# Optimization experiments

Measured on AMD Instinct MI355X. Metric: run time of the kernel, lower is better.

## Reference

```python
import jax, jax.numpy as jnp
import numpy as np
import math

DIM = 512
HEADS = 8
DH = DIM // HEADS          # 64 = dim_head
M = 17                     # num_landmarks
PINV_ITERS = 6
RES_K = 33                 # residual depthwise conv kernel (lucidrains default)


def layer_norm(x, g, b, eps=1e-5):
    mu = x.mean(-1, keepdims=True)
    var = ((x - mu) ** 2).mean(-1, keepdims=True)
    return (x - mu) * jax.lax.rsqrt(var + eps) * g + b


def dwconv2d(x, w, b, k):
    # x: [B,C,H,W], w: [C,1,k,k] depthwise
    p = k // 2
    y = jax.lax.conv_general_dilated(x, w, (1, 1), ((p, p), (p, p)),
        dimension_numbers=('NCHW', 'OIHW', 'NCHW'), feature_group_count=x.shape[1])
    return y + b[None, :, None, None]


def moore_penrose_pinv(x, iters=PINV_ITERS):
    ax = jnp.abs(x)
    z = jnp.swapaxes(x, -1, -2) / (jnp.max(ax.sum(-1)) * jnp.max(ax.sum(-2)))
    I = jnp.eye(x.shape[-1], dtype=x.dtype)
    for _ in range(iters):
        xz = x @ z
        z = 0.25 * z @ (13 * I - xz @ (15 * I - xz @ (7 * I - xz)))
    return z


def nystrom_attn(x, qkv_w, out_w, out_b, res_w):
    # lucidrains NystromAttention, eval mode (dropout=identity), return_attn=True
    b, n, _ = x.shape
    pad = (M - n % M) % M
    xp = jnp.pad(x, ((0, 0), (pad, 0), (0, 0)))  # pad at FRONT
    q, k, v = jnp.split(xp @ qkv_w, 3, axis=-1)
    to_heads = lambda t: t.reshape(b, -1, HEADS, DH).transpose(0, 2, 1, 3)  # b h n d
    q, k, v = to_heads(q), to_heads(k), to_heads(v)
    q = q * (DH ** -0.5)
    l = (n + pad) // M
    ql = q.reshape(b, HEADS, M, l, DH).mean(3)  # landmarks b h m d
    kl = k.reshape(b, HEADS, M, l, DH).mean(3)
    a1 = jax.nn.softmax(jnp.einsum('bhid,bhjd->bhij', q, kl), axis=-1)   # [b,h,n,m]
    a2 = jax.nn.softmax(jnp.einsum('bhid,bhjd->bhij', ql, kl), axis=-1)  # [b,h,m,m]
    a3 = jax.nn.softmax(jnp.einsum('bhid,bhjd->bhij', ql, k), axis=-1)   # [b,h,m,n]
    a2i = moore_penrose_pinv(a2)
    left = a1 @ a2i                       # [b,h,n,m]
    out = left @ (a3 @ v)                 # [b,h,n,d]
    # residual depthwise conv over heads, kernel (33,1) along seq
    res = jax.lax.conv_general_dilated(v, res_w, (1, 1), ((RES_K // 2, RES_K // 2), (0, 0)),
        dimension_numbers=('NCHW', 'OIHW', 'NCHW'), feature_group_count=HEADS)
    out = out + res
    out = out.transpose(0, 2, 1, 3).reshape(b, -1, DIM)
    out = out @ out_w + out_b
    attn = left @ a3                      # [b,h,n_pad,n_pad]
    return out[:, -n:], attn


def ppeg(x, H, W, w7, b7, w5, b5, w3, b3):
    B, _, C = x.shape
    cls_t, feat = x[:, :1], x[:, 1:]
    cnn = feat.transpose(0, 2, 1).reshape(B, C, H, W)
    y = dwconv2d(cnn, w7, b7, 7) + cnn + dwconv2d(cnn, w5, b5, 5) + dwconv2d(cnn, w3, b3, 3)
    y = y.reshape(B, C, H * W).transpose(0, 2, 1)
    return jnp.concatenate([cls_t, y], axis=1)


def setup_inputs():
    key = jax.random.key(0)
    ks = jax.random.split(key, 20)
    B, N, IN, NC = 2, 2048, 1024, 2
    s = 0.02
    d = {}
    d['feats'] = jax.random.normal(ks[0], (B, N, IN), jnp.float32)
    d['fc1_w'] = jax.random.normal(ks[1], (IN, DIM), jnp.float32) * s
    d['fc1_b'] = jnp.zeros((DIM,), jnp.float32)
    d['cls_token'] = jax.random.normal(ks[2], (1, 1, DIM), jnp.float32)
    for i, pre in enumerate(['l1', 'l2']):
        o = 3 + i * 3
        d[pre + '_norm_g'] = jnp.ones((DIM,), jnp.float32)
        d[pre + '_norm_b'] = jnp.zeros((DIM,), jnp.float32)
        d[pre + '_qkv_w'] = jax.random.normal(ks[o], (DIM, 3 * DIM), jnp.float32) * s
        d[pre + '_out_w'] = jax.random.normal(ks[o + 1], (DIM, DIM), jnp.float32) * s
        d[pre + '_out_b'] = jnp.zeros((DIM,), jnp.float32)
        d[pre + '_res_w'] = jax.random.normal(ks[o + 2], (HEADS, 1, RES_K, 1), jnp.float32) * s
    for kk, kidx in zip([7, 5, 3], [9, 10, 11]):
        d['ppeg_w%d' % kk] = jax.random.normal(ks[kidx], (DIM, 1, kk, kk), jnp.float32) * s
        d['ppeg_b%d' % kk] = jnp.zeros((DIM,), jnp.float32)
    d['norm_g'] = jnp.ones((DIM,), jnp.float32)
    d['norm_b'] = jnp.zeros((DIM,), jnp.float32)
    d['fc2_w'] = jax.random.normal(ks[12], (DIM, NC), jnp.float32) * s
    d['fc2_b'] = jnp.zeros((NC,), jnp.float32)
    return d


def reference(feats, fc1_w, fc1_b, cls_token,
              l1_norm_g, l1_norm_b, l1_qkv_w, l1_out_w, l1_out_b, l1_res_w,
              l2_norm_g, l2_norm_b, l2_qkv_w, l2_out_w, l2_out_b, l2_res_w,
              ppeg_w7, ppeg_b7, ppeg_w5, ppeg_b5, ppeg_w3, ppeg_b3,
              norm_g, norm_b, fc2_w, fc2_b):
    h = jax.nn.relu(feats @ fc1_w + fc1_b)          # [B,N,512]
    N = h.shape[1]
    Hs = int(math.ceil(math.sqrt(N)))               # square grid side
    add = Hs * Hs - N
    h = jnp.concatenate([h, h[:, :add]], axis=1)    # duplicate-pad to Hs*Hs
    B = h.shape[0]
    h = jnp.concatenate([jnp.broadcast_to(cls_token, (B, 1, DIM)), h], axis=1)
    a1, aw1 = nystrom_attn(layer_norm(h, l1_norm_g, l1_norm_b), l1_qkv_w, l1_out_w, l1_out_b, l1_res_w)
    h = h + a1
    h = ppeg(h, Hs, Hs, ppeg_w7, ppeg_b7, ppeg_w5, ppeg_b5, ppeg_w3, ppeg_b3)
    a2, aw2 = nystrom_attn(layer_norm(h, l2_norm_g, l2_norm_b), l2_qkv_w, l2_out_w, l2_out_b, l2_res_w)
    h = h + a2
    h = layer_norm(h, norm_g, norm_b)[:, 0]
    logits = h @ fc2_w + fc2_b
    return logits, aw1, aw2
```

## Files before the change

### kernel.cpp

```cpp
#include <hip/hip_runtime.h>
#include <math.h>
#include <stdint.h>

#define BATCH 2
#define NIN   1024
#define NSEQ  2048
#define DIMC  512
#define NH    8
#define DHD   64
#define MLM   17
#define LBLK  125
#define SEQ   2117
#define NPAD  2125
#define PAD0  8
#define HS    46
#define NPIX  2116
#define RA    4250
#define AWSZ  ((size_t)BATCH*NH*NPAD*NPAD)

typedef _Float16 half8 __attribute__((ext_vector_type(8)));
typedef float    floatx4 __attribute__((ext_vector_type(4)));

__device__ __forceinline__ void store_hl(_Float16* __restrict__ xh, _Float16* __restrict__ xl,
                                         int c, int ra, float v)
{
    _Float16 hv = (_Float16)v;
    size_t o = ((size_t)(c >> 3) * RA + ra) * 8 + (c & 7);
    xh[o] = hv;
    xl[o] = (_Float16)(v - (float)hv);
}

__global__ void convA_kernel(const float* __restrict__ X, _Float16* __restrict__ hi,
                             _Float16* __restrict__ lo, int R, int K)
{
    int GK = K >> 3;
    size_t idx = (size_t)blockIdx.x * 256 + threadIdx.x;
    if (idx >= (size_t)R * GK) return;
    int r = (int)(idx % R); int gk = (int)(idx / R);
    const float* s = X + (size_t)r * K + gk * 8;
    half8 h, l;
    #pragma unroll
    for (int j = 0; j < 8; ++j) {
        float x = s[j];
        _Float16 hh = (_Float16)x;
        h[j] = hh;
        l[j] = (_Float16)(x - (float)hh);
    }
    *(half8*)(hi + idx * 8) = h;
    *(half8*)(lo + idx * 8) = l;
}

__global__ void convB_kernel(const float* __restrict__ X, _Float16* __restrict__ hi,
                             _Float16* __restrict__ lo, int N, int K)
{
    int GK = K >> 3;
    size_t idx = (size_t)blockIdx.x * 256 + threadIdx.x;
    if (idx >= (size_t)N * GK) return;
    int n = (int)(idx % N); int gk = (int)(idx / N);
    const float* s = X + (size_t)(gk * 8) * N + n;
    half8 h, l;
    #pragma unroll
    for (int j = 0; j < 8; ++j) {
        float x = s[(size_t)j * N];
        _Float16 hh = (_Float16)x;
        h[j] = hh;
        l[j] = (_Float16)(x - (float)hh);
    }
    *(half8*)(hi + idx * 8) = h;
    *(half8*)(lo + idx * 8) = l;
}

__global__ __launch_bounds__(256) void gemm_mfma(
    const _Float16* __restrict__ Ah, const _Float16* __restrict__ Al,
    const _Float16* __restrict__ Bh, const _Float16* __restrict__ Bl,
    const float* __restrict__ bias, float* __restrict__ C,
    int Mn, int Nn, int Kn, int relu)
{
    __shared__ _Float16 sA[2][4][128][8];
    __shared__ _Float16 sB[2][4][128][8];
    const int tid = threadIdx.x;
    const int wv = tid >> 6, ln = tid & 63;
    const int m0 = blockIdx.y * 128, n0 = blockIdx.x * 128;
    const int wm = (wv >> 1) * 64, wn = (wv & 1) * 64;
    const int g = ln >> 4, rr = ln & 15;

    floatx4 acc[4][4];
    #pragma unroll
    for (int m = 0; m < 4; ++m)
        #pragma unroll
        for (int n = 0; n < 4; ++n)
            acc[m][n] = (floatx4){0.f, 0.f, 0.f, 0.f};

    for (int k0 = 0; k0 < Kn; k0 += 32) {
        int gk0 = k0 >> 3;
        #pragma unroll
        for (int q2 = 0; q2 < 8; ++q2) {
            int c = wv + q2 * 4;
            int arr = c >> 3, gg = (c >> 1) & 3, hf = c & 1;
            const _Float16* base = (arr == 0) ? Ah : (arr == 1) ? Al : (arr == 2) ? Bh : Bl;
            int Rdim = (arr < 2) ? Mn : Nn;
            int rg = ((arr < 2) ? m0 : n0) + hf * 64 + ln;
            if (arr < 2 && rg >= Mn) rg = Mn - 1;
            const _Float16* src = base + ((size_t)(gk0 + gg) * Rdim + rg) * 8;
            _Float16* dst = (arr == 0) ? &sA[0][gg][hf * 64][0] :
                            (arr == 1) ? &sA[1][gg][hf * 64][0] :
                            (arr == 2) ? &sB[0][gg][hf * 64][0] :
                                         &sB[1][gg][hf * 64][0];
            __builtin_amdgcn_global_load_lds(
                (__attribute__((address_space(1))) void*)(uintptr_t)src,
                (__attribute__((address_space(3))) void*)dst, 16, 0, 0);
        }
        __syncthreads();

        half8 a_h[4], a_l[4], b_h[4], b_l[4];
        #pragma unroll
        for (int m = 0; m < 4; ++m) {
            a_h[m] = *(const half8*)&sA[0][g][wm + m * 16 + rr][0];
            a_l[m] = *(const half8*)&sA[1][g][wm + m * 16 + rr][0];
        }
        #pragma unroll
        for (int n = 0; n < 4; ++n) {
            b_h[n] = *(const half8*)&sB[0][g][wn + n * 16 + rr][0];
            b_l[n] = *(const half8*)&sB[1][g][wn + n * 16 + rr][0];
        }
        #pragma unroll
        for (int m = 0; m < 4; ++m)
            #pragma unroll
            for (int n = 0; n < 4; ++n) {
                acc[m][n] = __builtin_amdgcn_mfma_f32_16x16x32_f16(a_h[m], b_h[n], acc[m][n], 0, 0, 0);
                acc[m][n] = __builtin_amdgcn_mfma_f32_16x16x32_f16(a_l[m], b_h[n], acc[m][n], 0, 0, 0);
                acc[m][n] = __builtin_amdgcn_mfma_f32_16x16x32_f16(a_h[m], b_l[n], acc[m][n], 0, 0, 0);
            }
        __syncthreads();
    }

    const int rq = ln >> 4;
    #pragma unroll
    for (int n = 0; n < 4; ++n) {
        int col = n0 + wn + n * 16 + rr;
        float bv = bias ? bias[col] : 0.f;
        #pragma unroll
        for (int m = 0; m < 4; ++m) {
            #pragma unroll
            for (int r = 0; r < 4; ++r) {
                int row = m0 + wm + m * 16 + rq * 4 + r;
                if (row < Mn) {
                    float vv = acc[m][n][r] + bv;
                    if (relu) vv = fmaxf(vv, 0.f);
                    C[(size_t)row * Nn + col] = vv;
                }
            }
        }
    }
}

__global__ void buildh_kernel(const float* __restrict__ h0, const float* __restrict__ cls,
                              float* __restrict__ h)
{
    size_t e = (size_t)blockIdx.x*256 + threadIdx.x;
    if (e >= (size_t)BATCH*SEQ*DIMC) return;
    int c = e % DIMC; size_t r = e / DIMC;
    int t = r % SEQ; int b = r / SEQ;
    float val;
    if (t == 0) val = cls[c];
    else {
        int n = t - 1;
        if (n >= NSEQ) n -= NSEQ;
        val = h0[((size_t)(b*NSEQ + n))*DIMC + c];
    }
    h[e] = val;
}

__global__ void ln_pad_kernel(const float* __restrict__ h, const float* __restrict__ g,
                              const float* __restrict__ bta,
                              _Float16* __restrict__ xh, _Float16* __restrict__ xl)
{
    int r = blockIdx.x; int b = blockIdx.y; int t = threadIdx.x;
    int ra = b*NPAD + r;
    if (r < PAD0) {
        store_hl(xh, xl, t, ra, 0.f);
        store_hl(xh, xl, t + 256, ra, 0.f);
        return;
    }
    const float* x = &h[((size_t)(b*SEQ + r-PAD0))*DIMC];
    __shared__ float red[256];
    float x0 = x[t], x1 = x[t+256];
    red[t] = x0 + x1; __syncthreads();
    for (int s=128;s>0;s>>=1){ if(t<s) red[t]+=red[t+s]; __syncthreads(); }
    float mu = red[0] * (1.f/512.f); __syncthreads();
    float d0 = x0-mu, d1 = x1-mu;
    red[t] = d0*d0 + d1*d1; __syncthreads();
    for (int s=128;s>0;s>>=1){ if(t<s) red[t]+=red[t+s]; __syncthreads(); }
    float rstd = 1.0f / sqrtf(red[0]*(1.f/512.f) + 1e-5f);
    store_hl(xh, xl, t,       ra, d0*rstd*g[t]     + bta[t]);
    store_hl(xh, xl, t + 256, ra, d1*rstd*g[t+256] + bta[t+256]);
}

__global__ void split_heads_kernel(const float* __restrict__ qkv, float* __restrict__ q,
                                   float* __restrict__ k, float* __restrict__ v)
{
    size_t idx = (size_t)blockIdx.x*256 + threadIdx.x;
    if (idx >= (size_t)BATCH*NH*NPAD*DHD) return;
    int d = idx % DHD; size_t r = idx / DHD;
    int i = r % NPAD; r /= NPAD;
    int h = r % NH; int b = r / NH;
    size_t src = ((size_t)(b*NPAD + i))*1536 + h*DHD + d;
    q[idx] = qkv[src] * 0.125f;
    k[idx] = qkv[src + 512];
    v[idx] = qkv[src + 1024];
}

__global__ void landmark_kernel(const float* __restrict__ q, const float* __restrict__ k,
                                float* __restrict__ ql, float* __restrict__ kl)
{
    int m = blockIdx.x, h = blockIdx.y, b = blockIdx.z, d = threadIdx.x;
    int bh = b*NH + h;
    size_t base = ((size_t)bh*NPAD + m*LBLK)*DHD + d;
    float sq = 0.f, sk = 0.f;
    for (int r=0;r<LBLK;++r){ sq += q[base + (size_t)r*DHD]; sk += k[base + (size_t)r*DHD]; }
    size_t o = ((size_t)bh*MLM + m)*DHD + d;
    ql[o] = sq / 125.f; kl[o] = sk / 125.f;
}

__global__ void a1_kernel(const float* __restrict__ q, const float* __restrict__ kl,
                          float* __restrict__ a1)
{
    int i = blockIdx.x, h = blockIdx.y, b = blockIdx.z;
    int bh = b*NH + h; int lane = threadIdx.x;
    __shared__ float qrow[64];
    __shared__ float dots[MLM];
    qrow[lane] = q[((size_t)bh*NPAD + i)*DHD + lane];
    __syncthreads();
    if (lane < MLM) {
        const float* krow = &kl[((size_t)bh*MLM + lane)*DHD];
        float acc = 0.f;
        for (int d=0; d<DHD; ++d) acc += qrow[d]*krow[d];
        dots[lane] = acc;
    }
    __syncthreads();
    if (lane < MLM) {
        float mx = -1e30f;
        for (int u=0;u<MLM;++u) mx = fmaxf(mx, dots[u]);
        float s = 0.f;
        for (int u=0;u<MLM;++u) s += expf(dots[u]-mx);
        a1[((size_t)bh*NPAD + i)*MLM + lane] = expf(dots[lane]-mx)/s;
    }
}

__global__ void a2_kernel(const float* __restrict__ ql, const float* __restrict__ kl,
                          float* __restrict__ a2)
{
    int bh = blockIdx.x; int t = threadIdx.x;
    __shared__ float s[MLM*MLM];
    if (t < MLM*MLM) {
        int m = t/MLM, j = t%MLM;
        const float* qr = &ql[((size_t)bh*MLM+m)*DHD];
        const float* kr = &kl[((size_t)bh*MLM+j)*DHD];
        float acc=0.f; for(int d=0;d<DHD;++d) acc += qr[d]*kr[d];
        s[t] = acc;
    }
    __syncthreads();
    if (t < MLM*MLM) {
        int m = t/MLM;
        float mx=-1e30f; for(int u=0;u<MLM;++u) mx=fmaxf(mx, s[m*MLM+u]);
        float sm=0.f; for(int u=0;u<MLM;++u) sm += expf(s[m*MLM+u]-mx);
        a2[(size_t)bh*MLM*MLM + t] = expf(s[t]-mx)/sm;
    }
}

__global__ void a3_kernel(const float* __restrict__ ql, const float* __restrict__ k,
                          float* __restrict__ a3)
{
    int m = blockIdx.x, h = blockIdx.y, b = blockIdx.z;
    int bh = b*NH + h; int tid = threadIdx.x;
    __shared__ float qlrow[64];
    __shared__ float buf[NPAD];
    __shared__ float red[256];
    if (tid < 64) qlrow[tid] = ql[((size_t)bh*MLM+m)*DHD + tid];
    __syncthreads();
    for (int j = tid; j < NPAD; j += 256) {
        const float* kr = &k[((size_t)bh*NPAD + j)*DHD];
        float acc = 0.f;
        for (int d=0; d<DHD; ++d) acc += qlrow[d]*kr[d];
        buf[j] = acc;
    }
    __syncthreads();
    float mx = -1e30f;
    for (int j = tid; j < NPAD; j += 256) mx = fmaxf(mx, buf[j]);
    red[tid] = mx; __syncthreads();
    for (int s=128;s>0;s>>=1){ if(tid<s) red[tid]=fmaxf(red[tid],red[tid+s]); __syncthreads(); }
    mx = red[0]; __syncthreads();
    float sm = 0.f;
    for (int j = tid; j < NPAD; j += 256) sm += expf(buf[j]-mx);
    red[tid] = sm; __syncthreads();
    for (int s=128;s>0;s>>=1){ if(tid<s) red[tid]+=red[tid+s]; __syncthreads(); }
    sm = red[0];
    for (int j = tid; j < NPAD; j += 256)
        a3[((size_t)bh*MLM+m)*NPAD + j] = expf(buf[j]-mx)/sm;
}

__global__ void pinv_scale_kernel(const float* __restrict__ a2, float* __restrict__ scal)
{
    int t = threadIdx.x;
    __shared__ float red[512];
    float rs = -1e30f, cs = -1e30f;
    if (t < BATCH*NH*MLM) {
        int bh = t/MLM, i = t%MLM;
        const float* x = &a2[(size_t)bh*MLM*MLM];
        float r=0.f, c=0.f;
        for (int j=0;j<MLM;++j){ r += fabsf(x[i*MLM+j]); c += fabsf(x[j*MLM+i]); }
        rs = r; cs = c;
    }
    red[t] = rs; __syncthreads();
    for (int s=256;s>0;s>>=1){ if(t<s) red[t]=fmaxf(red[t],red[t+s]); __syncthreads(); }
    float m1 = red[0]; __syncthreads();
    red[t] = cs; __syncthreads();
    for (int s=256;s>0;s>>=1){ if(t<s) red[t]=fmaxf(red[t],red[t+s]); __syncthreads(); }
    if (t==0) scal[0] = 1.f/(m1*red[0]);
}

__global__ void pinv_kernel(const float* __restrict__ a2, const float* __restrict__ scal,
                            float* __restrict__ a2i)
{
    int bh = blockIdx.x; int t = threadIdx.x;
    __shared__ float x[289], z[289], xz[289], w1[289], w2[289];
    int i = t/MLM, j = t%MLM;
    bool act = t < MLM*MLM;
    if (act) x[t] = a2[(size_t)bh*MLM*MLM + t];
    __syncthreads();
    if (act) z[t] = x[j*MLM+i] * scal[0];
    __syncthreads();
    for (int it=0; it<6; ++it) {
        if (act){ float a=0.f; for(int k2=0;k2<MLM;++k2) a += x[i*MLM+k2]*z[k2*MLM+j]; xz[t]=a; }
        __syncthreads();
        if (act){ w1[t] = (i==j?7.f:0.f) - xz[t]; }
        __syncthreads();
        if (act){ float a=0.f; for(int k2=0;k2<MLM;++k2) a += xz[i*MLM+k2]*w1[k2*MLM+j]; w2[t]=a; }
        __syncthreads();
        if (act){ w1[t] = (i==j?15.f:0.f) - w2[t]; }
        __syncthreads();
        if (act){ float a=0.f; for(int k2=0;k2<MLM;++k2) a += xz[i*MLM+k2]*w1[k2*MLM+j]; w2[t]=a; }
        __syncthreads();
        if (act){ w1[t] = (i==j?13.f:0.f) - w2[t]; }
        __syncthreads();
        if (act){ float a=0.f; for(int k2=0;k2<MLM;++k2) a += z[i*MLM+k2]*w1[k2*MLM+j]; w2[t]=0.25f*a; }
        __syncthreads();
        if (act) z[t] = w2[t];
        __syncthreads();
    }
    if (act) a2i[(size_t)bh*MLM*MLM + t] = z[t];
}

__global__ void left_kernel(const float* __restrict__ a1, const float* __restrict__ a2i,
                            float* __restrict__ left)
{
    int bh = blockIdx.z*NH + blockIdx.y;
    __shared__ float zi[289];
    int t = threadIdx.x;
    for (int u=t; u<289; u+=256) zi[u] = a2i[(size_t)bh*289+u];
    __syncthreads();
    int e = blockIdx.x*256 + t;
    if (e < NPAD*MLM) {
        int i = e/MLM, j = e%MLM;
        const float* ar = &a1[((size_t)bh*NPAD + i)*MLM];
        float acc=0.f;
        for (int k2=0;k2<MLM;++k2) acc += ar[k2]*zi[k2*MLM+j];
        left[((size_t)bh*NPAD+i)*MLM + j] = acc;
    }
}

__global__ void a3v_kernel(const float* __restrict__ a3, const float* __restrict__ v,
                           float* __restrict__ a3v)
{
    int m = blockIdx.x, h = blockIdx.y, b = blockIdx.z, d = threadIdx.x;
    int bh = b*NH + h;
    const float* ar = &a3[((size_t)bh*MLM+m)*NPAD];
    const float* vb = &v[(size_t)bh*NPAD*DHD + d];
    float acc = 0.f;
    for (int j=0;j<NPAD;++j) acc += ar[j]*vb[(size_t)j*DHD];
    a3v[((size_t)bh*MLM+m)*DHD + d] = acc;
}

__global__ void headout_kernel(const float* __restrict__ left, const float* __restrict__ a3v,
                               const float* __restrict__ v, const float* __restrict__ res_w,
                               _Float16* __restrict__ hh, _Float16* __restrict__ hl)
{
    int i = blockIdx.x, h = blockIdx.y, b = blockIdx.z, t = threadIdx.x;
    int bh = b*NH + h;
    __shared__ float lrow[MLM];
    __shared__ float rw[33];
    if (t < MLM) lrow[t] = left[((size_t)bh*NPAD+i)*MLM+t];
    if (t < 33)  rw[t] = res_w[h*33 + t];
    __syncthreads();
    float acc = 0.f;
    for (int m2=0;m2<MLM;++m2) acc += lrow[m2]*a3v[((size_t)bh*MLM+m2)*DHD+t];
    for (int s=0;s<33;++s) {
        int ii = i + s - 16;
        if (ii >= 0 && ii < NPAD) acc += rw[s]*v[((size_t)bh*NPAD+ii)*DHD+t];
    }
    store_hl(hh, hl, h*DHD + t, b*NPAD + i, acc);
}

__global__ __launch_bounds__(256) void attn_out_kernel(const float* __restrict__ left,
                                                       const float* __restrict__ a3,
                                                       float* __restrict__ aw)
{
    int bh = blockIdx.z; int i0 = blockIdx.y*64; int j0 = blockIdx.x*512;
    int t = threadIdx.x;
    __shared__ float lrows[64][20];
    for (int u = t; u < 64*MLM; u += 256) {
        int ii = u / MLM, kk = u % MLM;
        int gi = i0 + ii;
        lrows[ii][kk] = (gi < NPAD) ? left[((size_t)bh*NPAD + gi)*MLM + kk] : 0.f;
    }
    __syncthreads();
    int j1 = j0 + t, j2 = j0 + 256 + t;
    float c1[MLM], c2[MLM];
    #pragma unroll
    for (int kk = 0; kk < MLM; ++kk) {
        c1[kk] = (j1 < NPAD) ? a3[((size_t)bh*MLM + kk)*NPAD + j1] : 0.f;
        c2[kk] = (j2 < NPAD) ? a3[((size_t)bh*MLM + kk)*NPAD + j2] : 0.f;
    }
    int imax = NPAD - i0; if (imax > 64) imax = 64;
    for (int ii = 0; ii < imax; ++ii) {
        float lv[17];
        *(float4*)&lv[0]  = *(const float4*)&lrows[ii][0];
        *(float4*)&lv[4]  = *(const float4*)&lrows[ii][4];
        *(float4*)&lv[8]  = *(const float4*)&lrows[ii][8];
        *(float4*)&lv[12] = *(const float4*)&lrows[ii][12];
        lv[16] = lrows[ii][16];
        float s1 = 0.f, s2 = 0.f;
        #pragma unroll
        for (int kk = 0; kk < MLM; ++kk) { s1 += lv[kk]*c1[kk]; s2 += lv[kk]*c2[kk]; }
        size_t ob = ((size_t)bh*NPAD + (i0+ii))*NPAD;
        if (j1 < NPAD) aw[ob + j1] = s1;
        if (j2 < NPAD) aw[ob + j2] = s2;
    }
}

__global__ void add_res_kernel(float* __restrict__ h, const float* __restrict__ proj)
{
    size_t e = (size_t)blockIdx.x*256 + threadIdx.x;
    if (e >= (size_t)BATCH*SEQ*DIMC) return;
    int c = e % DIMC; size_t r = e / DIMC;
    int tt = r % SEQ; int b = r / SEQ;
    h[e] += proj[((size_t)(b*NPAD + PAD0 + tt))*DIMC + c];
}

__global__ void ppeg_im_kernel(const float* __restrict__ h, float* __restrict__ im)
{
    size_t e = (size_t)blockIdx.x*256 + threadIdx.x;
    if (e >= (size_t)BATCH*DIMC*NPIX) return;
    int p = e % NPIX; size_t r = e / NPIX;
    int c = r % DIMC; int b = r / DIMC;
    im[e] = h[((size_t)(b*SEQ) + 1 + p)*DIMC + c];
}

__global__ void ppeg_conv_kernel(const float* __restrict__ im,
                                 const float* __restrict__ w7, const float* __restrict__ b7,
                                 const float* __restrict__ w5, const float* __restrict__ b5,
                                 const float* __restrict__ w3, const float* __restrict__ b3,
                                 float* __restrict__ h)
{
    int c = blockIdx.x; int b = blockIdx.y; int t = threadIdx.x;
    __shared__ float img[NPIX];
    __shared__ float wf[49+25+9];
    const float* src = &im[((size_t)(b*DIMC+c))*NPIX];
    for (int p=t; p<NPIX; p+=256) img[p] = src[p];
    if (t < 49) wf[t] = w7[c*49+t];
    else if (t >= 64 && t < 64+25) wf[49 + (t-64)] = w5[c*25 + (t-64)];
    else if (t >= 96 && t < 96+9)  wf[74 + (t-96)] = w3[c*9 + (t-96)];
    __syncthreads();
    float bias = b7[c] + b5[c] + b3[c];
    for (int p=t; p<NPIX; p+=256) {
        int y = p/HS, x = p%HS;
        float acc = img[p] + bias;
        for (int dy=-3; dy<=3; ++dy){ int yy=y+dy; if (yy<0||yy>=HS) continue;
            for (int dx=-3; dx<=3; ++dx){ int xx=x+dx; if (xx<0||xx>=HS) continue;
                acc += wf[(dy+3)*7+(dx+3)]*img[yy*HS+xx]; } }
        for (int dy=-2; dy<=2; ++dy){ int yy=y+dy; if (yy<0||yy>=HS) continue;
            for (int dx=-2; dx<=2; ++dx){ int xx=x+dx; if (xx<0||xx>=HS) continue;
                acc += wf[49+(dy+2)*5+(dx+2)]*img[yy*HS+xx]; } }
        for (int dy=-1; dy<=1; ++dy){ int yy=y+dy; if (yy<0||yy>=HS) continue;
            for (int dx=-1; dx<=1; ++dx){ int xx=x+dx; if (xx<0||xx>=HS) continue;
                acc += wf[74+(dy+1)*3+(dx+1)]*img[yy*HS+xx]; } }
        h[((size_t)(b*SEQ)+1+p)*DIMC + c] = acc;
    }
}

__global__ void final_kernel(const float* __restrict__ h, const float* __restrict__ g,
                             const float* __restrict__ bta, const float* __restrict__ fc2w,
                             const float* __restrict__ fc2b, float* __restrict__ out)
{
    int b = blockIdx.x; int t = threadIdx.x;
    __shared__ float red[512];
    const float* x = &h[(size_t)b*SEQ*DIMC];
    float xv = x[t];
    red[t] = xv; __syncthreads();
    for (int s=256;s>0;s>>=1){ if(t<s) red[t]+=red[t+s]; __syncthreads(); }
    float mu = red[0]/512.f; __syncthreads();
    float d = xv - mu;
    red[t] = d*d; __syncthreads();
    for (int s=256;s>0;s>>=1){ if(t<s) red[t]+=red[t+s]; __syncthreads(); }
    float var = red[0]/512.f; __syncthreads();
    float hn = d * (1.f/sqrtf(var+1e-5f)) * g[t] + bta[t];
    for (int c=0;c<2;++c) {
        red[t] = hn * fc2w[t*2+c]; __syncthreads();
        for (int s=256;s>0;s>>=1){ if(t<s) red[t]+=red[t+s]; __syncthreads(); }
        if (t==0) out[b*2+c] = red[0] + fc2b[c];
        __syncthreads();
    }
}

extern "C" void kernel_launch(void* const* d_in, const int* in_sizes, int n_in,
                              void* d_out, int out_size, void* d_ws, size_t ws_size,
                              hipStream_t stream)
{
    (void)in_sizes; (void)n_in; (void)out_size; (void)ws_size;
    const float* feats = (const float*)d_in[0];
    const float* fc1_w = (const float*)d_in[1];
    const float* fc1_b = (const float*)d_in[2];
    const float* cls   = (const float*)d_in[3];
    const float* ln_g[2]  = {(const float*)d_in[4],  (const float*)d_in[10]};
    const float* ln_b[2]  = {(const float*)d_in[5],  (const float*)d_in[11]};
    const float* qkv_w[2] = {(const float*)d_in[6],  (const float*)d_in[12]};
    const float* out_w[2] = {(const float*)d_in[7],  (const float*)d_in[13]};
    const float* out_b[2] = {(const float*)d_in[8],  (const float*)d_in[14]};
    const float* res_w[2] = {(const float*)d_in[9],  (const float*)d_in[15]};
    const float* w7 = (const float*)d_in[16]; const float* b7 = (const float*)d_in[17];
    const float* w5 = (const float*)d_in[18]; const float* b5 = (const float*)d_in[19];
    const float* w3 = (const float*)d_in[20]; const float* b3 = (const float*)d_in[21];
    const float* ng = (const float*)d_in[22]; const float* nb = (const float*)d_in[23];
    const float* fc2w = (const float*)d_in[24]; const float* fc2b = (const float*)d_in[25];

    float* ws = (float*)d_ws;
    size_t off = 0;
    float* h    = ws + off; off += (size_t)BATCH*SEQ*DIMC;
    float* h0   = ws + off; off += (size_t)BATCH*NSEQ*DIMC;
    float* qkv  = ws + off; off += (size_t)BATCH*NPAD*1536;
    float* q    = ws + off; off += (size_t)BATCH*NH*NPAD*DHD;
    float* k    = ws + off; off += (size_t)BATCH*NH*NPAD*DHD;
    float* v    = ws + off; off += (size_t)BATCH*NH*NPAD*DHD;
    float* ql   = ws + off; off += (size_t)BATCH*NH*MLM*DHD;
    float* kl   = ws + off; off += (size_t)BATCH*NH*MLM*DHD;
    float* a1   = ws + off; off += (size_t)BATCH*NH*NPAD*MLM;
    float* a2   = ws + off; off += (size_t)BATCH*NH*MLM*MLM;
    float* a2i  = ws + off; off += (size_t)BATCH*NH*MLM*MLM;
    float* scal = ws + off; off += 16;
    float* a3   = ws + off; off += (size_t)BATCH*NH*MLM*NPAD;
    float* left = ws + off; off += (size_t)BATCH*NH*NPAD*MLM;
    float* a3v  = ws + off; off += (size_t)BATCH*NH*MLM*DHD;
    _Float16* XAh = (_Float16*)(ws + off); off += 2097152;
    _Float16* XAl = (_Float16*)(ws + off); off += 2097152;
    _Float16* WBh = (_Float16*)(ws + off); off += 393216;
    _Float16* WBl = (_Float16*)(ws + off); off += 393216;
    float* proj = qkv;
    float* im   = qkv + (size_t)BATCH*NPAD*DIMC;

    float* outp = (float*)d_out;

    convA_kernel<<<((size_t)4096*128+255)/256, 256, 0, stream>>>(feats, XAh, XAl, 4096, NIN);
    convB_kernel<<<((size_t)512*128+255)/256, 256, 0, stream>>>(fc1_w, WBh, WBl, DIMC, NIN);
    gemm_mfma<<<dim3(DIMC/128, 4096/128), 256, 0, stream>>>(
        XAh, XAl, WBh, WBl, fc1_b, h0, BATCH*NSEQ, DIMC, NIN, 1);
    {
        size_t tot = (size_t)BATCH*SEQ*DIMC;
        buildh_kernel<<<(tot+255)/256, 256, 0, stream>>>(h0, cls, h);
    }

    for (int L = 0; L < 2; ++L) {
        float* aw = outp + 4 + (size_t)L*AWSZ;
        ln_pad_kernel<<<dim3(NPAD, BATCH), 256, 0, stream>>>(h, ln_g[L], ln_b[L], XAh, XAl);
        convB_kernel<<<((size_t)1536*64+255)/256, 256, 0, stream>>>(qkv_w[L], WBh, WBl, 1536, DIMC);
        gemm_mfma<<<dim3(1536/128, (RA+127)/128), 256, 0, stream>>>(
            XAh, XAl, WBh, WBl, nullptr, qkv, RA, 1536, DIMC, 0);
        {
            size_t tot = (size_t)BATCH*NH*NPAD*DHD;
            split_heads_kernel<<<(tot+255)/256, 256, 0, stream>>>(qkv, q, k, v);
        }
        landmark_kernel<<<dim3(MLM, NH, BATCH), 64, 0, stream>>>(q, k, ql, kl);
        a1_kernel<<<dim3(NPAD, NH, BATCH), 64, 0, stream>>>(q, kl, a1);
        a2_kernel<<<dim3(BATCH*NH), 320, 0, stream>>>(ql, kl, a2);
        a3_kernel<<<dim3(MLM, NH, BATCH), 256, 0, stream>>>(ql, k, a3);
        pinv_scale_kernel<<<1, 512, 0, stream>>>(a2, scal);
        pinv_kernel<<<BATCH*NH, 320, 0, stream>>>(a2, scal, a2i);
        left_kernel<<<dim3((NPAD*MLM+255)/256, NH, BATCH), 256, 0, stream>>>(a1, a2i, left);
        a3v_kernel<<<dim3(MLM, NH, BATCH), 64, 0, stream>>>(a3, v, a3v);
        headout_kernel<<<dim3(NPAD, NH, BATCH), 64, 0, stream>>>(left, a3v, v, res_w[L], XAh, XAl);
        attn_out_kernel<<<dim3((NPAD+511)/512, (NPAD+63)/64, BATCH*NH), 256, 0, stream>>>(left, a3, aw);
        convB_kernel<<<((size_t)512*64+255)/256, 256, 0, stream>>>(out_w[L], WBh, WBl, DIMC, DIMC);
        gemm_mfma<<<dim3(DIMC/128, (RA+127)/128), 256, 0, stream>>>(
            XAh, XAl, WBh, WBl, out_b[L], proj, RA, DIMC, DIMC, 0);
        {
            size_t tot = (size_t)BATCH*SEQ*DIMC;
            add_res_kernel<<<(tot+255)/256, 256, 0, stream>>>(h, proj);
        }
        if (L == 0) {
            size_t tot = (size_t)BATCH*DIMC*NPIX;
            ppeg_im_kernel<<<(tot+255)/256, 256, 0, stream>>>(h, im);
            ppeg_conv_kernel<<<dim3(DIMC, BATCH), 256, 0, stream>>>(im, w7, b7, w5, b5, w3, b3, h);
        }
    }
    final_kernel<<<BATCH, 512, 0, stream>>>(h, ng, nb, fc2w, fc2b, outp);
}
```

Measured before the change: 1.404 ms.

## Double-buffer GEMM, fuse head split and a1/left, tile-transpose PPEG, vectorize kernels

```diff
diff --git a/kernel.cpp b/kernel.cpp
--- a/kernel.cpp
+++ b/kernel.cpp
@@ -74,10 +74,11 @@
     const _Float16* __restrict__ Ah, const _Float16* __restrict__ Al,
     const _Float16* __restrict__ Bh, const _Float16* __restrict__ Bl,
     const float* __restrict__ bias, float* __restrict__ C,
-    int Mn, int Nn, int Kn, int relu)
-{
-    __shared__ _Float16 sA[2][4][128][8];
-    __shared__ _Float16 sB[2][4][128][8];
+    int Mn, int Nn, int Kn, int relu,
+    int split, float* __restrict__ qp, float* __restrict__ kp, float* __restrict__ vp)
+{
+    __shared__ _Float16 sA[2][2][4][128][8];
+    __shared__ _Float16 sB[2][2][4][128][8];
     const int tid = threadIdx.x;
     const int wv = tid >> 6, ln = tid & 63;
     const int m0 = blockIdx.y * 128, n0 = blockIdx.x * 128;
@@ -91,8 +92,7 @@
         for (int n = 0; n < 4; ++n)
             acc[m][n] = (floatx4){0.f, 0.f, 0.f, 0.f};
 
-    for (int k0 = 0; k0 < Kn; k0 += 32) {
-        int gk0 = k0 >> 3;
+    auto STAGE = [&](int bf, int gk0) {
         #pragma unroll
         for (int q2 = 0; q2 < 8; ++q2) {
             int c = wv + q2 * 4;
@@ -102,26 +102,32 @@
             int rg = ((arr < 2) ? m0 : n0) + hf * 64 + ln;
             if (arr < 2 && rg >= Mn) rg = Mn - 1;
             const _Float16* src = base + ((size_t)(gk0 + gg) * Rdim + rg) * 8;
-            _Float16* dst = (arr == 0) ? &sA[0][gg][hf * 64][0] :
-                            (arr == 1) ? &sA[1][gg][hf * 64][0] :
-                            (arr == 2) ? &sB[0][gg][hf * 64][0] :
-                                         &sB[1][gg][hf * 64][0];
+            _Float16* dst = (arr == 0) ? &sA[bf][0][gg][hf * 64][0] :
+                            (arr == 1) ? &sA[bf][1][gg][hf * 64][0] :
+                            (arr == 2) ? &sB[bf][0][gg][hf * 64][0] :
+                                         &sB[bf][1][gg][hf * 64][0];
             __builtin_amdgcn_global_load_lds(
                 (__attribute__((address_space(1))) void*)(uintptr_t)src,
                 (__attribute__((address_space(3))) void*)dst, 16, 0, 0);
         }
-        __syncthreads();
-
+    };
+
+    const int nt = Kn >> 5;
+    STAGE(0, 0);
+    __syncthreads();
+    for (int t = 0; t < nt; ++t) {
+        const int cur = t & 1;
+        if (t + 1 < nt) STAGE(cur ^ 1, (t + 1) * 4);
         half8 a_h[4], a_l[4], b_h[4], b_l[4];
         #pragma unroll
         for (int m = 0; m < 4; ++m) {
-            a_h[m] = *(const half8*)&sA[0][g][wm + m * 16 + rr][0];
-            a_l[m] = *(const half8*)&sA[1][g][wm + m * 16 + rr][0];
+            a_h[m] = *(const half8*)&sA[cur][0][g][wm + m * 16 + rr][0];
+            a_l[m] = *(const half8*)&sA[cur][1][g][wm + m * 16 + rr][0];
         }
         #pragma unroll
         for (int n = 0; n < 4; ++n) {
-            b_h[n] = *(const half8*)&sB[0][g][wn + n * 16 + rr][0];
-            b_l[n] = *(const half8*)&sB[1][g][wn + n * 16 + rr][0];
+            b_h[n] = *(const half8*)&sB[cur][0][g][wn + n * 16 + rr][0];
+            b_l[n] = *(const half8*)&sB[cur][1][g][wn + n * 16 + rr][0];
         }
         #pragma unroll
         for (int m = 0; m < 4; ++m)
@@ -135,40 +141,62 @@
     }
 
     const int rq = ln >> 4;
-    #pragma unroll
-    for (int n = 0; n < 4; ++n) {
-        int col = n0 + wn + n * 16 + rr;
-        float bv = bias ? bias[col] : 0.f;
-        #pragma unroll
-        for (int m = 0; m < 4; ++m) {
+    if (!split) {
+        #pragma unroll
+        for (int n = 0; n < 4; ++n) {
+            int col = n0 + wn + n * 16 + rr;
+            float bv = bias ? bias[col] : 0.f;
             #pragma unroll
-            for (int r = 0; r < 4; ++r) {
-                int row = m0 + wm + m * 16 + rq * 4 + r;
-                if (row < Mn) {
-                    float vv = acc[m][n][r] + bv;
-                    if (relu) vv = fmaxf(vv, 0.f);
-                    C[(size_t)row * Nn + col] = vv;
+            for (int m = 0; m < 4; ++m) {
+                #pragma unroll
+                for (int r = 0; r < 4; ++r) {
+                    int row = m0 + wm + m * 16 + rq * 4 + r;
+                    if (row < Mn) {
+                        float vv = acc[m][n][r] + bv;
+                        if (relu) vv = fmaxf(vv, 0.f);
+                        C[(size_t)row * Nn + col] = vv;
+                    }
                 }
             }
         }
+    } else {
+        #pragma unroll
+        for (int n = 0; n < 4; ++n) {
+            int col = n0 + wn + n * 16 + rr;
+            int sect = col >> 9, hh = (col >> 6) & 7, dd = col & 63;
+            float* dstb = (sect == 0) ? qp : (sect == 1) ? kp : vp;
+            float sc = (sect == 0) ? 0.125f : 1.f;
+            #pragma unroll
+            for (int m = 0; m < 4; ++m) {
+                #pragma unroll
+                for (int r = 0; r < 4; ++r) {
+                    int row = m0 + wm + m * 16 + rq * 4 + r;
+                    if (row < Mn) {
+                        int b = (row >= NPAD) ? 1 : 0;
+                        int i = row - b * NPAD;
+                        dstb[(((size_t)(b * NH + hh)) * NPAD + i) * DHD + dd] = acc[m][n][r] * sc;
+                    }
+                }
+            }
+        }
     }
 }
 
 __global__ void buildh_kernel(const float* __restrict__ h0, const float* __restrict__ cls,
                               float* __restrict__ h)
 {
-    size_t e = (size_t)blockIdx.x*256 + threadIdx.x;
-    if (e >= (size_t)BATCH*SEQ*DIMC) return;
-    int c = e % DIMC; size_t r = e / DIMC;
-    int t = r % SEQ; int b = r / SEQ;
-    float val;
-    if (t == 0) val = cls[c];
+    size_t e4 = (size_t)blockIdx.x*256 + threadIdx.x;
+    if (e4 >= (size_t)BATCH*SEQ*DIMC/4) return;
+    int c4 = (int)(e4 % (DIMC/4)); size_t r = e4 / (DIMC/4);
+    int t = (int)(r % SEQ); int b = (int)(r / SEQ);
+    float4 val;
+    if (t == 0) val = ((const float4*)cls)[c4];
     else {
         int n = t - 1;
         if (n >= NSEQ) n -= NSEQ;
-        val = h0[((size_t)(b*NSEQ + n))*DIMC + c];
-    }
-    h[e] = val;
+        val = ((const float4*)h0)[((size_t)(b*NSEQ + n))*(DIMC/4) + c4];
+    }
+    ((float4*)h)[e4] = val;
 }
 
 __global__ void ln_pad_kernel(const float* __restrict__ h, const float* __restrict__ g,
@@ -183,31 +211,25 @@
         return;
     }
     const float* x = &h[((size_t)(b*SEQ + r-PAD0))*DIMC];
-    __shared__ float red[256];
+    __shared__ float ws[4];
+    int wid = t >> 6, ln = t & 63;
     float x0 = x[t], x1 = x[t+256];
-    red[t] = x0 + x1; __syncthreads();
-    for (int s=128;s>0;s>>=1){ if(t<s) red[t]+=red[t+s]; __syncthreads(); }
-    float mu = red[0] * (1.f/512.f); __syncthreads();
+    float s = x0 + x1;
+    #pragma unroll
+    for (int m = 1; m < 64; m <<= 1) s += __shfl_xor(s, m, 64);
+    if (ln == 0) ws[wid] = s;
+    __syncthreads();
+    float mu = (ws[0]+ws[1]+ws[2]+ws[3]) * (1.f/512.f);
     float d0 = x0-mu, d1 = x1-mu;
-    red[t] = d0*d0 + d1*d1; __syncthreads();
-    for (int s=128;s>0;s>>=1){ if(t<s) red[t]+=red[t+s]; __syncthreads(); }
-    float rstd = 1.0f / sqrtf(red[0]*(1.f/512.f) + 1e-5f);
+    float vv = d0*d0 + d1*d1;
+    #pragma unroll
+    for (int m = 1; m < 64; m <<= 1) vv += __shfl_xor(vv, m, 64);
+    __syncthreads();
+    if (ln == 0) ws[wid] = vv;
+    __syncthreads();
+    float rstd = 1.0f / sqrtf((ws[0]+ws[1]+ws[2]+ws[3])*(1.f/512.f) + 1e-5f);
     store_hl(xh, xl, t,       ra, d0*rstd*g[t]     + bta[t]);
     store_hl(xh, xl, t + 256, ra, d1*rstd*g[t+256] + bta[t+256]);
-}
-
-__global__ void split_heads_kernel(const float* __restrict__ qkv, float* __restrict__ q,
-                                   float* __restrict__ k, float* __restrict__ v)
-{
-    size_t idx = (size_t)blockIdx.x*256 + threadIdx.x;
-    if (idx >= (size_t)BATCH*NH*NPAD*DHD) return;
-    int d = idx % DHD; size_t r = idx / DHD;
-    int i = r % NPAD; r /= NPAD;
-    int h = r % NH; int b = r / NH;
-    size_t src = ((size_t)(b*NPAD + i))*1536 + h*DHD + d;
-    q[idx] = qkv[src] * 0.125f;
-    k[idx] = qkv[src + 512];
-    v[idx] = qkv[src + 1024];
 }
 
 __global__ void landmark_kernel(const float* __restrict__ q, const float* __restrict__ k,
@@ -222,19 +244,25 @@
     ql[o] = sq / 125.f; kl[o] = sk / 125.f;
 }
 
-__global__ void a1_kernel(const float* __restrict__ q, const float* __restrict__ kl,
-                          float* __restrict__ a1)
+__global__ void a1_left_kernel(const float* __restrict__ q, const float* __restrict__ kl,
+                               const float* __restrict__ a2i, float* __restrict__ left)
 {
     int i = blockIdx.x, h = blockIdx.y, b = blockIdx.z;
     int bh = b*NH + h; int lane = threadIdx.x;
-    __shared__ float qrow[64];
+    __shared__ alignas(16) float qrow[64];
     __shared__ float dots[MLM];
+    __shared__ float arow[MLM];
     qrow[lane] = q[((size_t)bh*NPAD + i)*DHD + lane];
     __syncthreads();
     if (lane < MLM) {
-        const float* krow = &kl[((size_t)bh*MLM + lane)*DHD];
+        const float4* kr4 = (const float4*)&kl[((size_t)bh*MLM + lane)*DHD];
+        const float4* q4 = (const float4*)qrow;
         float acc = 0.f;
-        for (int d=0; d<DHD; ++d) acc += qrow[d]*krow[d];
+        #pragma unroll
+        for (int d4=0; d4<16; ++d4) {
+            float4 a = q4[d4], bb = kr4[d4];
+            acc += a.x*bb.x + a.y*bb.y + a.z*bb.z + a.w*bb.w;
+        }
         dots[lane] = acc;
     }
     __syncthreads();
@@ -243,7 +271,14 @@
         for (int u=0;u<MLM;++u) mx = fmaxf(mx, dots[u]);
         float s = 0.f;
         for (int u=0;u<MLM;++u) s += expf(dots[u]-mx);
-        a1[((size_t)bh*NPAD + i)*MLM + lane] = expf(dots[lane]-mx)/s;
+        arow[lane] = expf(dots[lane]-mx)/s;
+    }
+    __syncthreads();
+    if (lane < MLM) {
+        const float* zi = &a2i[(size_t)bh*MLM*MLM];
+        float acc = 0.f;
+        for (int k2=0;k2<MLM;++k2) acc += arow[k2]*zi[k2*MLM + lane];
+        left[((size_t)bh*NPAD + i)*MLM + lane] = acc;
     }
 }
 
@@ -273,15 +308,20 @@
 {
     int m = blockIdx.x, h = blockIdx.y, b = blockIdx.z;
     int bh = b*NH + h; int tid = threadIdx.x;
-    __shared__ float qlrow[64];
+    __shared__ alignas(16) float qlrow[64];
     __shared__ float buf[NPAD];
     __shared__ float red[256];
     if (tid < 64) qlrow[tid] = ql[((size_t)bh*MLM+m)*DHD + tid];
     __syncthreads();
     for (int j = tid; j < NPAD; j += 256) {
-        const float* kr = &k[((size_t)bh*NPAD + j)*DHD];
+        const float4* kr4 = (const float4*)&k[((size_t)bh*NPAD + j)*DHD];
+        const float4* q4 = (const float4*)qlrow;
         float acc = 0.f;
-        for (int d=0; d<DHD; ++d) acc += qlrow[d]*kr[d];
+        #pragma unroll
+        for (int d4=0; d4<16; ++d4) {
+            float4 kk = kr4[d4], qq = q4[d4];
+            acc += qq.x*kk.x + qq.y*kk.y + qq.z*kk.z + qq.w*kk.w;
+        }
         buf[j] = acc;
     }
     __syncthreads();
@@ -299,36 +339,31 @@
         a3[((size_t)bh*MLM+m)*NPAD + j] = expf(buf[j]-mx)/sm;
 }
 
-__global__ void pinv_scale_kernel(const float* __restrict__ a2, float* __restrict__ scal)
-{
-    int t = threadIdx.x;
-    __shared__ float red[512];
+__global__ void pinv_kernel(const float* __restrict__ a2, float* __restrict__ a2i)
+{
+    int bh = blockIdx.x; int t = threadIdx.x;
+    __shared__ float x[289], z[289], xz[289], w1[289], w2[289];
+    __shared__ float red[320], red2[320];
     float rs = -1e30f, cs = -1e30f;
     if (t < BATCH*NH*MLM) {
-        int bh = t/MLM, i = t%MLM;
-        const float* x = &a2[(size_t)bh*MLM*MLM];
+        int m2 = t/MLM, i2 = t%MLM;
+        const float* xx = &a2[(size_t)m2*MLM*MLM];
         float r=0.f, c=0.f;
-        for (int j=0;j<MLM;++j){ r += fabsf(x[i*MLM+j]); c += fabsf(x[j*MLM+i]); }
+        for (int j=0;j<MLM;++j){ r += fabsf(xx[i2*MLM+j]); c += fabsf(xx[j*MLM+i2]); }
         rs = r; cs = c;
     }
-    red[t] = rs; __syncthreads();
-    for (int s=256;s>0;s>>=1){ if(t<s) red[t]=fmaxf(red[t],red[t+s]); __syncthreads(); }
-    float m1 = red[0]; __syncthreads();
-    red[t] = cs; __syncthreads();
-    for (int s=256;s>0;s>>=1){ if(t<s) red[t]=fmaxf(red[t],red[t+s]); __syncthreads(); }
-    if (t==0) scal[0] = 1.f/(m1*red[0]);
-}
-
-__global__ void pinv_kernel(const float* __restrict__ a2, const float* __restrict__ scal,
-                            float* __restrict__ a2i)
-{
-    int bh = blockIdx.x; int t = threadIdx.x;
-    __shared__ float x[289], z[289], xz[289], w1[289], w2[289];
+    red[t] = rs; red2[t] = cs; __syncthreads();
+    for (int s=256;s>0;s>>=1){
+        if (t<s && t+s<320){ red[t]=fmaxf(red[t],red[t+s]); red2[t]=fmaxf(red2[t],red2[t+s]); }
+        __syncthreads();
+    }
+    float scal = 1.f/(red[0]*red2[0]);
+
     int i = t/MLM, j = t%MLM;
     bool act = t < MLM*MLM;
     if (act) x[t] = a2[(size_t)bh*MLM*MLM + t];
     __syncthreads();
-    if (act) z[t] = x[j*MLM+i] * scal[0];
+    if (act) z[t] = x[j*MLM+i] * scal;
     __syncthreads();
     for (int it=0; it<6; ++it) {
         if (act){ float a=0.f; for(int k2=0;k2<MLM;++k2) a += x[i*MLM+k2]*z[k2*MLM+j]; xz[t]=a; }
@@ -349,24 +384,6 @@
         __syncthreads();
     }
     if (act) a2i[(size_t)bh*MLM*MLM + t] = z[t];
-}
-
-__global__ void left_kernel(const float* __restrict__ a1, const float* __restrict__ a2i,
-                            float* __restrict__ left)
-{
-    int bh = blockIdx.z*NH + blockIdx.y;
-    __shared__ float zi[289];
-    int t = threadIdx.x;
-    for (int u=t; u<289; u+=256) zi[u] = a2i[(size_t)bh*289+u];
-    __syncthreads();
-    int e = blockIdx.x*256 + t;
-    if (e < NPAD*MLM) {
-        int i = e/MLM, j = e%MLM;
-        const float* ar = &a1[((size_t)bh*NPAD + i)*MLM];
-        float acc=0.f;
-        for (int k2=0;k2<MLM;++k2) acc += ar[k2]*zi[k2*MLM+j];
-        left[((size_t)bh*NPAD+i)*MLM + j] = acc;
-    }
 }
 
 __global__ void a3v_kernel(const float* __restrict__ a3, const float* __restrict__ v,
@@ -440,27 +457,40 @@
 
 __global__ void add_res_kernel(float* __restrict__ h, const float* __restrict__ proj)
 {
-    size_t e = (size_t)blockIdx.x*256 + threadIdx.x;
-    if (e >= (size_t)BATCH*SEQ*DIMC) return;
-    int c = e % DIMC; size_t r = e / DIMC;
-    int tt = r % SEQ; int b = r / SEQ;
-    h[e] += proj[((size_t)(b*NPAD + PAD0 + tt))*DIMC + c];
-}
-
-__global__ void ppeg_im_kernel(const float* __restrict__ h, float* __restrict__ im)
-{
-    size_t e = (size_t)blockIdx.x*256 + threadIdx.x;
-    if (e >= (size_t)BATCH*DIMC*NPIX) return;
-    int p = e % NPIX; size_t r = e / NPIX;
-    int c = r % DIMC; int b = r / DIMC;
-    im[e] = h[((size_t)(b*SEQ) + 1 + p)*DIMC + c];
+    size_t e4 = (size_t)blockIdx.x*256 + threadIdx.x;
+    if (e4 >= (size_t)BATCH*SEQ*DIMC/4) return;
+    int c4 = (int)(e4 % (DIMC/4)); size_t r = e4 / (DIMC/4);
+    int tt = (int)(r % SEQ); int b = (int)(r / SEQ);
+    float4 p = ((const float4*)proj)[((size_t)(b*NPAD + PAD0 + tt))*(DIMC/4) + c4];
+    float4* hp = &((float4*)h)[e4];
+    float4 hv = *hp;
+    hv.x += p.x; hv.y += p.y; hv.z += p.z; hv.w += p.w;
+    *hp = hv;
+}
+
+__global__ void transpose_h2im(const float* __restrict__ h, float* __restrict__ im)
+{
+    __shared__ float tile[32][33];
+    int p0 = blockIdx.x*32, c0 = blockIdx.y*32, b = blockIdx.z;
+    int tx = threadIdx.x & 31, ty = threadIdx.x >> 5;
+    #pragma unroll
+    for (int i=0;i<32;i+=8) {
+        int p = p0 + ty + i;
+        if (p < NPIX) tile[ty+i][tx] = h[((size_t)(b*SEQ) + 1 + p)*DIMC + c0 + tx];
+    }
+    __syncthreads();
+    #pragma unroll
+    for (int i=0;i<32;i+=8) {
+        int c = c0 + ty + i, p = p0 + tx;
+        if (p < NPIX) im[((size_t)(b*DIMC) + c)*NPIX + p] = tile[tx][ty+i];
+    }
 }
 
 __global__ void ppeg_conv_kernel(const float* __restrict__ im,
                                  const float* __restrict__ w7, const float* __restrict__ b7,
                                  const float* __restrict__ w5, const float* __restrict__ b5,
                                  const float* __restrict__ w3, const float* __restrict__ b3,
-                                 float* __restrict__ h)
+                                 float* __restrict__ im2)
 {
     int c = blockIdx.x; int b = blockIdx.y; int t = threadIdx.x;
     __shared__ float img[NPIX];
@@ -484,7 +514,25 @@
         for (int dy=-1; dy<=1; ++dy){ int yy=y+dy; if (yy<0||yy>=HS) continue;
             for (int dx=-1; dx<=1; ++dx){ int xx=x+dx; if (xx<0||xx>=HS) continue;
                 acc += wf[74+(dy+1)*3+(dx+1)]*img[yy*HS+xx]; } }
-        h[((size_t)(b*SEQ)+1+p)*DIMC + c] = acc;
+        im2[((size_t)(b*DIMC)+c)*NPIX + p] = acc;
+    }
+}
+
+__global__ void transpose_im2h(const float* __restrict__ im2, float* __restrict__ h)
+{
+    __shared__ float tile[32][33];
+    int p0 = blockIdx.x*32, c0 = blockIdx.y*32, b = blockIdx.z;
+    int tx = threadIdx.x & 31, ty = threadIdx.x >> 5;
+    #pragma unroll
+    for (int i=0;i<32;i+=8) {
+        int c = c0 + ty + i, p = p0 + tx;
+        if (p < NPIX) tile[ty+i][tx] = im2[((size_t)(b*DIMC) + c)*NPIX + p];
+    }
+    __syncthreads();
+    #pragma unroll
+    for (int i=0;i<32;i+=8) {
+        int p = p0 + ty + i;
+        if (p < NPIX) h[((size_t)(b*SEQ) + 1 + p)*DIMC + c0 + tx] = tile[tx][ty+i];
     }
 }
 
@@ -537,16 +585,14 @@
     size_t off = 0;
     float* h    = ws + off; off += (size_t)BATCH*SEQ*DIMC;
     float* h0   = ws + off; off += (size_t)BATCH*NSEQ*DIMC;
-    float* qkv  = ws + off; off += (size_t)BATCH*NPAD*1536;
+    float* scr  = ws + off; off += (size_t)BATCH*NPAD*1536;
     float* q    = ws + off; off += (size_t)BATCH*NH*NPAD*DHD;
     float* k    = ws + off; off += (size_t)BATCH*NH*NPAD*DHD;
     float* v    = ws + off; off += (size_t)BATCH*NH*NPAD*DHD;
     float* ql   = ws + off; off += (size_t)BATCH*NH*MLM*DHD;
     float* kl   = ws + off; off += (size_t)BATCH*NH*MLM*DHD;
-    float* a1   = ws + off; off += (size_t)BATCH*NH*NPAD*MLM;
-    float* a2   = ws + off; off += (size_t)BATCH*NH*MLM*MLM;
-    float* a2i  = ws + off; off += (size_t)BATCH*NH*MLM*MLM;
-    float* scal = ws + off; off += 16;
+    float* a2   = ws + off; off += (size_t)BATCH*NH*MLM*MLM + 15;
+    float* a2i  = ws + off; off += (size_t)BATCH*NH*MLM*MLM + 15;
     float* a3   = ws + off; off += (size_t)BATCH*NH*MLM*NPAD;
     float* left = ws + off; off += (size_t)BATCH*NH*NPAD*MLM;
     float* a3v  = ws + off; off += (size_t)BATCH*NH*MLM*DHD;
@@ -554,18 +600,19 @@
     _Float16* XAl = (_Float16*)(ws + off); off += 2097152;
     _Float16* WBh = (_Float16*)(ws + off); off += 393216;
     _Float16* WBl = (_Float16*)(ws + off); off += 393216;
-    float* proj = qkv;
-    float* im   = qkv + (size_t)BATCH*NPAD*DIMC;
+    float* proj = scr;
+    float* im   = scr + (size_t)BATCH*NPAD*DIMC;
+    float* im2  = im  + (size_t)BATCH*DIMC*NPIX;
 
     float* outp = (float*)d_out;
 
     convA_kernel<<<((size_t)4096*128+255)/256, 256, 0, stream>>>(feats, XAh, XAl, 4096, NIN);
     convB_kernel<<<((size_t)512*128+255)/256, 256, 0, stream>>>(fc1_w, WBh, WBl, DIMC, NIN);
     gemm_mfma<<<dim3(DIMC/128, 4096/128), 256, 0, stream>>>(
-        XAh, XAl, WBh, WBl, fc1_b, h0, BATCH*NSEQ, DIMC, NIN, 1);
+        XAh, XAl, WBh, WBl, fc1_b, h0, BATCH*NSEQ, DIMC, NIN, 1, 0, nullptr, nullptr, nullptr);
     {
-        size_t tot = (size_t)BATCH*SEQ*DIMC;
-        buildh_kernel<<<(tot+255)/256, 256, 0, stream>>>(h0, cls, h);
+        size_t tot4 = (size_t)BATCH*SEQ*DIMC/4;
+        buildh_kernel<<<(tot4+255)/256, 256, 0, stream>>>(h0, cls, h);
     }
 
     for (int L = 0; L < 2; ++L) {
@@ -573,32 +620,26 @@
         ln_pad_kernel<<<dim3(NPAD, BATCH), 256, 0, stream>>>(h, ln_g[L], ln_b[L], XAh, XAl);
         convB_kernel<<<((size_t)1536*64+255)/256, 256, 0, stream>>>(qkv_w[L], WBh, WBl, 1536, DIMC);
         gemm_mfma<<<dim3(1536/128, (RA+127)/128), 256, 0, stream>>>(
-            XAh, XAl, WBh, WBl, nullptr, qkv, RA, 1536, DIMC, 0);
-        {
-            size_t tot = (size_t)BATCH*NH*NPAD*DHD;
-            split_heads_kernel<<<(tot+255)/256, 256, 0, stream>>>(qkv, q, k, v);
-        }
+            XAh, XAl, WBh, WBl, nullptr, nullptr, RA, 1536, DIMC, 0, 1, q, k, v);
         landmark_kernel<<<dim3(MLM, NH, BATCH), 64, 0, stream>>>(q, k, ql, kl);
-        a1_kernel<<<dim3(NPAD, NH, BATCH), 64, 0, stream>>>(q, kl, a1);
         a2_kernel<<<dim3(BATCH*NH), 320, 0, stream>>>(ql, kl, a2);
         a3_kernel<<<dim3(MLM, NH, BATCH), 256, 0, stream>>>(ql, k, a3);
-        pinv_scale_kernel<<<1, 512, 0, stream>>>(a2, scal);
-        pinv_kernel<<<BATCH*NH, 320, 0, stream>>>(a2, scal, a2i);
-        left_kernel<<<dim3((NPAD*MLM+255)/256, NH, BATCH), 256, 0, stream>>>(a1, a2i, left);
+        pinv_kernel<<<BATCH*NH, 320, 0, stream>>>(a2, a2i);
+        a1_left_kernel<<<dim3(NPAD, NH, BATCH), 64, 0, stream>>>(q, kl, a2i, left);
         a3v_kernel<<<dim3(MLM, NH, BATCH), 64, 0, stream>>>(a3, v, a3v);
         headout_kernel<<<dim3(NPAD, NH, BATCH), 64, 0, stream>>>(left, a3v, v, res_w[L], XAh, XAl);
         attn_out_kernel<<<dim3((NPAD+511)/512, (NPAD+63)/64, BATCH*NH), 256, 0, stream>>>(left, a3, aw);
         convB_kernel<<<((size_t)512*64+255)/256, 256, 0, stream>>>(out_w[L], WBh, WBl, DIMC, DIMC);
         gemm_mfma<<<dim3(DIMC/128, (RA+127)/128), 256, 0, stream>>>(
-            XAh, XAl, WBh, WBl, out_b[L], proj, RA, DIMC, DIMC, 0);
+            XAh, XAl, WBh, WBl, out_b[L], proj, RA, DIMC, DIMC, 0, 0, nullptr, nullptr, nullptr);
         {
-            size_t tot = (size_t)BATCH*SEQ*DIMC;
-            add_res_kernel<<<(tot+255)/256, 256, 0, stream>>>(h, proj);
+            size_t tot4 = (size_t)BATCH*SEQ*DIMC/4;
+            add_res_kernel<<<(tot4+255)/256, 256, 0, stream>>>(h, proj);
         }
         if (L == 0) {
-            size_t tot = (size_t)BATCH*DIMC*NPIX;
-            ppeg_im_kernel<<<(tot+255)/256, 256, 0, stream>>>(h, im);
-            ppeg_conv_kernel<<<dim3(DIMC, BATCH), 256, 0, stream>>>(im, w7, b7, w5, b5, w3, b3, h);
+            transpose_h2im<<<dim3((NPIX+31)/32, DIMC/32, BATCH), 256, 0, stream>>>(h, im);
+            ppeg_conv_kernel<<<dim3(DIMC, BATCH), 256, 0, stream>>>(im, w7, b7, w5, b5, w3, b3, im2);
+            transpose_im2h<<<dim3((NPIX+31)/32, DIMC/32, BATCH), 256, 0, stream>>>(im2, h);
         }
     }
     final_kernel<<<BATCH, 512, 0, stream>>>(h, ng, nb, fc2w, fc2b, outp);
```

After: 1.364 ms. 1.03x faster.
